# Kernel optimization log

Measured on AMD Instinct MI355X. Metric: run time of the kernel, lower is better.

The kernel has to match this reference:

```python
import jax, jax.numpy as jnp
import numpy as np

# LLRDenoiser config (init_kwargs): ndim=2, patch W=8, stride S=4, ths=0.1, rand_shift=False
P = 8      # patch size (isotropic)
STRIDE = 4 # patch stride
THS = 0.1  # soft-threshold on singular values
B, C, H, W = 2, 16, 512, 512  # batch, coefficient axis, spatial dims


def setup_inputs() -> dict:
    key = jax.random.key(0)
    x = jax.random.normal(key, (B, C, H, W), dtype=jnp.float32)
    return {"x": x}


def _patch_idx(n, p, s):
    # start indices for sliding windows, inclusive of last full window
    starts = jnp.arange(0, n - p + 1, s)
    return starts[:, None] + jnp.arange(p)[None, :]  # (n_patches, p)


def _llr_denoise(x):
    idx_h = _patch_idx(H, P, STRIDE)  # (nH, P)
    idx_w = _patch_idx(W, P, STRIDE)  # (nW, P)
    nH, nW = idx_h.shape[0], idx_w.shape[0]
    hi = idx_h[:, None, :, None]  # (nH, 1, P, 1)
    wi = idx_w[None, :, None, :]  # (1, nW, 1, P)

    # extract overlapping patches -> (B, C, nH, nW, P, P)
    patches = x[:, :, hi, wi]
    # Casorati matrices per patch: (B, nH*nW, C, P*P)
    mats = patches.transpose(0, 2, 3, 1, 4, 5).reshape(B, nH * nW, C, P * P)

    # batched thin SVD + soft-threshold of singular values
    u, s, vh = jnp.linalg.svd(mats, full_matrices=False)
    s_st = jnp.sign(s) * jnp.maximum(jnp.abs(s) - THS, 0.0)
    mats = (u * s_st[..., None, :]) @ vh

    # back to patch layout (B, C, nH, nW, P, P)
    patches = mats.reshape(B, nH, nW, C, P, P).transpose(0, 3, 1, 2, 4, 5)

    # overlap-add reconstruction, averaged by patch coverage count
    out = jnp.zeros_like(x).at[:, :, hi, wi].add(patches)
    cnt = jnp.zeros((H, W), x.dtype).at[hi[..., 0, :, :] if False else idx_h[:, None, :, None], idx_w[None, :, None, :]].add(1.0)
    return out / cnt


def reference(x):
    return _llr_denoise(x)
```

## Files before the change

kernel.cpp:

```cpp
#include <hip/hip_runtime.h>


#define NBATCH  2
#define NCH     16
#define HDIM    512
#define WDIM    512
#define NPH     127
#define NPW     127
#define NPATCH  (NBATCH * NPH * NPW)
#define NCELL   128
#define THS     0.1f
#define NSIT    8

typedef short bf16x8 __attribute__((ext_vector_type(8)));
typedef float f32x4  __attribute__((ext_vector_type(4)));

#define MFMA(a,b,c) __builtin_amdgcn_mfma_f32_16x16x32_bf16((a),(b),(c),0,0,0)

static __device__ inline short f2bf(float x) {
  return __builtin_bit_cast(short, (__bf16)x);
}
static __device__ inline float blo2f(unsigned int v) {
  return __builtin_bit_cast(float, v << 16);
}
static __device__ inline float bhi2f(unsigned int v) {
  return __builtin_bit_cast(float, v & 0xffff0000u);
}
static __device__ inline unsigned int pack2bf(float lo, float hi) {
  unsigned int a = (unsigned short)f2bf(lo);
  unsigned int b = (unsigned short)f2bf(hi);
  return (b << 16) | a;
}

static __device__ inline int xcd_swz(int b, int nwg) {
  const int q = nwg >> 3, r = nwg & 7;
  const int x = b & 7, lo = b >> 3;
  return (x < r ? x * (q + 1) : r * (q + 1) + (x - r) * q) + lo;
}

static __device__ inline bf16x8 fragc(f32x4 v) {
  bf16x8 r;
  r[0] = f2bf(v[0]); r[1] = f2bf(v[1]); r[2] = f2bf(v[2]); r[3] = f2bf(v[3]);
  r[4] = 0; r[5] = 0; r[6] = 0; r[7] = 0;
  return r;
}

#define ZS_NBLK ((NPATCH + 3) / 4)
__global__ __launch_bounds__(256) void llr_zs(const float* __restrict__ x,
                                              uint2* __restrict__ zs) {
  const int blk = xcd_swz(blockIdx.x, ZS_NBLK);
  const int pid = blk * 4 + (threadIdx.x >> 6);
  if (pid >= NPATCH) return;
  const int bi  = pid / (NPH * NPW);
  const int pr  = pid % (NPH * NPW);
  const int ph  = pr / NPW, pw = pr % NPW;
  const int h0  = ph * 4, w0 = pw * 4;
  const int l   = threadIdx.x & 63;
  const int j   = l & 15;
  const int u   = l >> 4;

  const size_t HW = (size_t)HDIM * WDIM;
  const float* xb = x + (size_t)bi * NCH * HW;

  const float* pb = xb + (size_t)j * HW + (size_t)h0 * WDIM + w0;
  const int dh0 = (u >> 1), dw0 = 4 * (u & 1);
  float4 q0 = *(const float4*)(pb + (size_t)(dh0 + 0) * WDIM + dw0);
  float4 q1 = *(const float4*)(pb + (size_t)(dh0 + 2) * WDIM + dw0);
  float4 q2 = *(const float4*)(pb + (size_t)(dh0 + 4) * WDIM + dw0);
  float4 q3 = *(const float4*)(pb + (size_t)(dh0 + 6) * WDIM + dw0);

  bf16x8 m0, m1;
  m0[0]=f2bf(q0.x); m0[1]=f2bf(q0.y); m0[2]=f2bf(q0.z); m0[3]=f2bf(q0.w);
  m0[4]=f2bf(q1.x); m0[5]=f2bf(q1.y); m0[6]=f2bf(q1.z); m0[7]=f2bf(q1.w);
  m1[0]=f2bf(q2.x); m1[1]=f2bf(q2.y); m1[2]=f2bf(q2.z); m1[3]=f2bf(q2.w);
  m1[4]=f2bf(q3.x); m1[5]=f2bf(q3.y); m1[6]=f2bf(q3.z); m1[7]=f2bf(q3.w);

  f32x4 g = {0.f, 0.f, 0.f, 0.f};
  g = MFMA(m0, m0, g);
  g = MFMA(m1, m1, g);

  float s2 = g[0]*g[0] + g[1]*g[1] + g[2]*g[2] + g[3]*g[3];
  #pragma unroll
  for (int m = 32; m >= 1; m >>= 1) s2 += __shfl_xor(s2, m, 64);

  uint2 wv = {0u, 0u};
  if (s2 > 1e-20f) {
    const float invf  = rsqrtf(s2);
    const float gsc   = 2.0f * invf;
    const float alpha = THS * sqrtf(gsc);

    f32x4 Yc, Zc;
    #pragma unroll
    for (int r = 0; r < 4; ++r) {
      Yc[r] = g[r] * gsc;
      Zc[r] = (4 * u + r == j) ? 1.0f : 0.0f;
    }

    const f32x4 zero = {0.f, 0.f, 0.f, 0.f};
    for (int it = 0; it < NSIT - 1; ++it) {
      bf16x8 yF = fragc(Yc), zF = fragc(Zc);
      f32x4 t  = MFMA(zF, yF, zero);
      bf16x8 tF = fragc(t);
      f32x4 py = MFMA(yF, tF, zero);
      f32x4 pz = MFMA(tF, zF, zero);
      #pragma unroll
      for (int r = 0; r < 4; ++r) {
        Yc[r] = 1.5f * Yc[r] - 0.5f * py[r];
        Zc[r] = 1.5f * Zc[r] - 0.5f * pz[r];
      }
    }
    {
      bf16x8 yF = fragc(Yc), zF = fragc(Zc);
      f32x4 t  = MFMA(zF, yF, zero);
      bf16x8 tF = fragc(t);
      f32x4 pz = MFMA(tF, zF, zero);
      #pragma unroll
      for (int r = 0; r < 4; ++r) Zc[r] = 1.5f * Zc[r] - 0.5f * pz[r];
    }

    wv.x = pack2bf(alpha * Zc[0], alpha * Zc[1]);
    wv.y = pack2bf(alpha * Zc[2], alpha * Zc[3]);
  }
  zs[(size_t)pid * 64 + l] = wv;
}

#define Q_NBLK (NBATCH * NCELL * 4)
__global__ __launch_bounds__(512, 8) void llr_q(const float* __restrict__ x,
                                                const uint2* __restrict__ zs,
                                                float* __restrict__ out) {
  __shared__ float RS[33 * 260];

  const int bid = blockIdx.x;
  const int qs  = bid & 3;
  const int ci  = (bid >> 2) & 127;
  const int bi  = bid >> 9;
  const int t   = threadIdx.x;
  const int r   = t >> 7;
  const int px  = t & 127;
  const int c   = px >> 2;

  const size_t HW = (size_t)HDIM * WDIM;
  const int h   = 4 * ci + r;
  const int wpx = qs * 128 + px;
  const float* xp = x + (size_t)bi * NCH * HW + (size_t)h * WDIM + wpx;

  float xv[16];
  #pragma unroll
  for (int e = 0; e < 16; ++e) xv[e] = xp[(size_t)e * HW];

  {
    const int w8 = t >> 6;
    const int l  = t & 63;
    const int u  = l >> 4, j = l & 15;
    const uint2* zb = zs + (size_t)bi * NPH * NPW * 64;
    const bool vh0 = (ci > 0), vh1 = (ci < NPH);
    const int ph0c = vh0 ? ci - 1 : 0;
    const int ph1c = vh1 ? ci : NPH - 1;
    for (int s = w8; s < 33; s += 8) {
      const int pw = qs * 32 - 1 + s;
      const bool vw = ((unsigned)pw <= (unsigned)(NPW - 1));
      const int pwc = vw ? pw : 0;
      uint2 z0 = zb[((size_t)ph0c * NPW + pwc) * 64 + l];
      uint2 z1 = zb[((size_t)ph1c * NPW + pwc) * 64 + l];
      if (!(vw && vh0)) { z0.x = 0u; z0.y = 0u; }
      if (!(vw && vh1)) { z1.x = 0u; z1.y = 0u; }
      float* rs = &RS[s * 260 + j];
      rs[16 * (4 * u + 0)] = blo2f(z0.x) + blo2f(z1.x);
      rs[16 * (4 * u + 1)] = bhi2f(z0.x) + bhi2f(z1.x);
      rs[16 * (4 * u + 2)] = blo2f(z0.y) + blo2f(z1.y);
      rs[16 * (4 * u + 3)] = bhi2f(z0.y) + bhi2f(z1.y);
    }
  }
  __syncthreads();

  const int cj = qs * 32 + c;
  const float cnth = 2.0f - (ci == 0) - (ci == NCELL - 1);
  const float cntw = 2.0f - (cj == 0) - (cj == NCELL - 1);
  const float sc = 1.0f / (cnth * cntw);

  const float* rsA = &RS[c * 260];
  const float* rsB = &RS[(c + 1) * 260];
  float* po = out + (size_t)bi * NCH * HW + (size_t)h * WDIM + wpx;
  #pragma unroll
  for (int co = 0; co < 16; ++co) {
    float acc = 0.f;
    #pragma unroll
    for (int k = 0; k < 4; ++k) {
      const float4 A = *(const float4*)(rsA + 16 * co + 4 * k);
      const float4 B = *(const float4*)(rsB + 16 * co + 4 * k);
      acc += (A.x + B.x) * xv[4 * k + 0];
      acc += (A.y + B.y) * xv[4 * k + 1];
      acc += (A.z + B.z) * xv[4 * k + 2];
      acc += (A.w + B.w) * xv[4 * k + 3];
    }
    po[(size_t)co * HW] = xv[co] - sc * acc;
  }
}

extern "C" void kernel_launch(void* const* d_in, const int* in_sizes, int n_in,
                              void* d_out, int out_size, void* d_ws, size_t ws_size,
                              hipStream_t stream) {
  const float* x = (const float*)d_in[0];
  float* out = (float*)d_out;
  uint2* zs = (uint2*)d_ws;

  llr_zs<<<dim3(ZS_NBLK), dim3(256), 0, stream>>>(x, zs);
  llr_q<<<dim3(Q_NBLK), dim3(512), 0, stream>>>(x, zs, out);
}
```

Measured before the change: 48.54 us.

## Pipeline per-batch zs and apply kernels with fused overlap launch and packed bf16 weights

Splits the work per batch so that computing batch 1's whitening matrices runs in the same launch as batch 0's apply stage (heterogeneous blocks in one fused kernel), with three launches total. The apply stage now pre-sums the two neighbouring patch matrices into a packed bf16 LDS table and computes all 16 outputs with one pass over the table instead of re-reading two float tables per output. This is meant to fill idle CUs across the stage boundary and cut LDS traffic. In exchange it adds a launch, an extra syncthreads, more LDS per block, and bf16 rounding of the summed weights.

Result: slower. 53.06 us (+9.3%).

```diff
diff --git a/kernel.cpp b/kernel.cpp
--- a/kernel.cpp
+++ b/kernel.cpp
@@ -7,10 +7,13 @@
 #define WDIM    512
 #define NPH     127
 #define NPW     127
-#define NPATCH  (NBATCH * NPH * NPW)
+#define NPB     (NPH * NPW)
 #define NCELL   128
 #define THS     0.1f
 #define NSIT    8
+
+#define ZS8_NBLK ((NPB + 7) / 8)
+#define APQ_NBLK (NCELL * 4)
 
 typedef short bf16x8 __attribute__((ext_vector_type(8)));
 typedef float f32x4  __attribute__((ext_vector_type(4)));
@@ -45,17 +48,16 @@
   return r;
 }
 
-#define ZS_NBLK ((NPATCH + 3) / 4)
-__global__ __launch_bounds__(256) void llr_zs(const float* __restrict__ x,
-                                              uint2* __restrict__ zs) {
-  const int blk = xcd_swz(blockIdx.x, ZS_NBLK);
-  const int pid = blk * 4 + (threadIdx.x >> 6);
-  if (pid >= NPATCH) return;
-  const int bi  = pid / (NPH * NPW);
-  const int pr  = pid % (NPH * NPW);
+static __device__ void zs_body(const float* __restrict__ x,
+                               uint2* __restrict__ zs,
+                               int zblk, int bi, int t) {
+  const int blk = xcd_swz(zblk, ZS8_NBLK);
+  const int pr  = blk * 8 + (t >> 6);
+  if (pr >= NPB) return;
+  const int pid = bi * NPB + pr;
   const int ph  = pr / NPW, pw = pr % NPW;
   const int h0  = ph * 4, w0 = pw * 4;
-  const int l   = threadIdx.x & 63;
+  const int l   = t & 63;
   const int j   = l & 15;
   const int u   = l >> 4;
 
@@ -99,8 +101,8 @@
     const f32x4 zero = {0.f, 0.f, 0.f, 0.f};
     for (int it = 0; it < NSIT - 1; ++it) {
       bf16x8 yF = fragc(Yc), zF = fragc(Zc);
-      f32x4 t  = MFMA(zF, yF, zero);
-      bf16x8 tF = fragc(t);
+      f32x4 tt = MFMA(zF, yF, zero);
+      bf16x8 tF = fragc(tt);
       f32x4 py = MFMA(yF, tF, zero);
       f32x4 pz = MFMA(tF, zF, zero);
       #pragma unroll
@@ -111,8 +113,8 @@
     }
     {
       bf16x8 yF = fragc(Yc), zF = fragc(Zc);
-      f32x4 t  = MFMA(zF, yF, zero);
-      bf16x8 tF = fragc(t);
+      f32x4 tt = MFMA(zF, yF, zero);
+      bf16x8 tF = fragc(tt);
       f32x4 pz = MFMA(tF, zF, zero);
       #pragma unroll
       for (int r = 0; r < 4; ++r) Zc[r] = 1.5f * Zc[r] - 0.5f * pz[r];
@@ -124,17 +126,13 @@
   zs[(size_t)pid * 64 + l] = wv;
 }
 
-#define Q_NBLK (NBATCH * NCELL * 4)
-__global__ __launch_bounds__(512, 8) void llr_q(const float* __restrict__ x,
-                                                const uint2* __restrict__ zs,
-                                                float* __restrict__ out) {
-  __shared__ float RS[33 * 260];
-
-  const int bid = blockIdx.x;
-  const int qs  = bid & 3;
-  const int ci  = (bid >> 2) & 127;
-  const int bi  = bid >> 9;
-  const int t   = threadIdx.x;
+static __device__ void apply_body(const float* __restrict__ x,
+                                  const uint2* __restrict__ zs,
+                                  float* __restrict__ out,
+                                  float* RS, unsigned int* PW,
+                                  int abid, int bi, int t) {
+  const int qs  = abid & 3;
+  const int ci  = abid >> 2;
   const int r   = t >> 7;
   const int px  = t & 127;
   const int c   = px >> 2;
@@ -152,7 +150,7 @@
     const int w8 = t >> 6;
     const int l  = t & 63;
     const int u  = l >> 4, j = l & 15;
-    const uint2* zb = zs + (size_t)bi * NPH * NPW * 64;
+    const uint2* zb = zs + (size_t)bi * NPB * 64;
     const bool vh0 = (ci > 0), vh1 = (ci < NPH);
     const int ph0c = vh0 ? ci - 1 : 0;
     const int ph1c = vh1 ? ci : NPH - 1;
@@ -173,27 +171,73 @@
   }
   __syncthreads();
 
+  {
+    const int cc = t >> 4, j = t & 15;
+    #pragma unroll
+    for (int m = 0; m < 8; ++m) {
+      const float lo = RS[cc * 260 + 32 * m + j]
+                     + RS[(cc + 1) * 260 + 32 * m + j];
+      const float hi = RS[cc * 260 + 32 * m + 16 + j]
+                     + RS[(cc + 1) * 260 + 32 * m + 16 + j];
+      PW[cc * 132 + 16 * m + j] = pack2bf(lo, hi);
+    }
+  }
+  __syncthreads();
+
   const int cj = qs * 32 + c;
   const float cnth = 2.0f - (ci == 0) - (ci == NCELL - 1);
   const float cntw = 2.0f - (cj == 0) - (cj == NCELL - 1);
   const float sc = 1.0f / (cnth * cntw);
 
-  const float* rsA = &RS[c * 260];
-  const float* rsB = &RS[(c + 1) * 260];
-  float* po = out + (size_t)bi * NCH * HW + (size_t)h * WDIM + wpx;
-  #pragma unroll
-  for (int co = 0; co < 16; ++co) {
-    float acc = 0.f;
+  float acc[16];
+  #pragma unroll
+  for (int co = 0; co < 16; ++co) acc[co] = 0.f;
+  #pragma unroll
+  for (int p = 0; p < 8; ++p) {
     #pragma unroll
     for (int k = 0; k < 4; ++k) {
-      const float4 A = *(const float4*)(rsA + 16 * co + 4 * k);
-      const float4 B = *(const float4*)(rsB + 16 * co + 4 * k);
-      acc += (A.x + B.x) * xv[4 * k + 0];
-      acc += (A.y + B.y) * xv[4 * k + 1];
-      acc += (A.z + B.z) * xv[4 * k + 2];
-      acc += (A.w + B.w) * xv[4 * k + 3];
-    }
-    po[(size_t)co * HW] = xv[co] - sc * acc;
+      const uint4 V = *(const uint4*)&PW[c * 132 + 16 * p + 4 * k];
+      const unsigned int vv[4] = {V.x, V.y, V.z, V.w};
+      #pragma unroll
+      for (int e2 = 0; e2 < 4; ++e2) {
+        const int e = 4 * k + e2;
+        acc[2 * p]     += blo2f(vv[e2]) * xv[e];
+        acc[2 * p + 1] += bhi2f(vv[e2]) * xv[e];
+      }
+    }
+  }
+
+  float* po = out + (size_t)bi * NCH * HW + (size_t)h * WDIM + wpx;
+  #pragma unroll
+  for (int co = 0; co < 16; ++co)
+    po[(size_t)co * HW] = xv[co] - sc * acc[co];
+}
+
+__global__ __launch_bounds__(512, 6) void llr_zs8(const float* __restrict__ x,
+                                                  uint2* __restrict__ zs,
+                                                  int bi) {
+  zs_body(x, zs, blockIdx.x, bi, threadIdx.x);
+}
+
+__global__ __launch_bounds__(512, 6) void llr_ap(const float* __restrict__ x,
+                                                 const uint2* __restrict__ zs,
+                                                 float* __restrict__ out,
+                                                 int bi) {
+  __shared__ float RS[33 * 260];
+  __shared__ unsigned int PW[32 * 132];
+  apply_body(x, zs, out, RS, PW, blockIdx.x, bi, threadIdx.x);
+}
+
+__global__ __launch_bounds__(512, 6) void llr_fused(const float* __restrict__ x,
+                                                    uint2* __restrict__ zs,
+                                                    float* __restrict__ out) {
+  __shared__ float RS[33 * 260];
+  __shared__ unsigned int PW[32 * 132];
+  const int bid = blockIdx.x;
+  if (bid < APQ_NBLK) {
+    apply_body(x, zs, out, RS, PW, bid, 0, threadIdx.x);
+  } else {
+    zs_body(x, zs, bid - APQ_NBLK, 1, threadIdx.x);
   }
 }
 
@@ -204,6 +248,7 @@
   float* out = (float*)d_out;
   uint2* zs = (uint2*)d_ws;
 
-  llr_zs<<<dim3(ZS_NBLK), dim3(256), 0, stream>>>(x, zs);
-  llr_q<<<dim3(Q_NBLK), dim3(512), 0, stream>>>(x, zs, out);
-}
+  llr_zs8<<<dim3(ZS8_NBLK), dim3(512), 0, stream>>>(x, zs, 0);
+  llr_fused<<<dim3(APQ_NBLK + ZS8_NBLK), dim3(512), 0, stream>>>(x, zs, out);
+  llr_ap<<<dim3(APQ_NBLK), dim3(512), 0, stream>>>(x, zs, out, 1);
+}
```
